# Optimization experiments

Measured on AMD Instinct MI355X. Metric: run time of the kernel, lower is better.

The kernel has to match this reference:

```python
import jax, jax.numpy as jnp
import numpy as np

EMBED_DIM = 1024
NUM_HEADS = 16
HEAD_DIM = EMBED_DIM // NUM_HEADS
B, S = 2, 2048


def setup_inputs() -> dict:
    key = jax.random.key(0)
    ks = jax.random.split(key, 11)
    glorot = lambda k, shape: jax.random.normal(k, shape, jnp.float32) * (2.0 / sum(shape)) ** 0.5
    return {
        "query": jax.random.normal(ks[0], (B, S, EMBED_DIM), jnp.float32),
        "key": jax.random.normal(ks[1], (B, S, EMBED_DIM), jnp.float32),
        "value": jax.random.normal(ks[2], (B, S, EMBED_DIM), jnp.float32),
        "Wq": glorot(ks[3], (EMBED_DIM, EMBED_DIM)), "bq": jnp.zeros((EMBED_DIM,), jnp.float32),
        "Wk": glorot(ks[4], (EMBED_DIM, EMBED_DIM)), "bk": jnp.zeros((EMBED_DIM,), jnp.float32),
        "Wv": glorot(ks[5], (EMBED_DIM, EMBED_DIM)), "bv": jnp.zeros((EMBED_DIM,), jnp.float32),
        "Wo": glorot(ks[6], (EMBED_DIM, EMBED_DIM)), "bo": jnp.zeros((EMBED_DIM,), jnp.float32),
    }


def reference(query, key, value, Wq, bq, Wk, bk, Wv, bv, Wo, bo):
    b, s, _ = query.shape
    # QKV projections
    q = query @ Wq + bq
    k = key @ Wk + bk
    v = value @ Wv + bv
    # [B, S, H, D] -> [B, H, S, D]
    q = q.reshape(b, s, NUM_HEADS, HEAD_DIM).transpose(0, 2, 1, 3)
    k = k.reshape(b, s, NUM_HEADS, HEAD_DIM).transpose(0, 2, 1, 3)
    v = v.reshape(b, s, NUM_HEADS, HEAD_DIM).transpose(0, 2, 1, 3)
    # scores [B, H, S, S], materialized as in the original
    scores = jnp.einsum("bhqd,bhkd->bhqk", q, k) / jnp.sqrt(jnp.float32(HEAD_DIM))
    attn = jax.nn.softmax(scores, axis=-1)
    out = jnp.einsum("bhqk,bhkd->bhqd", attn, v)  # [B, H, S, D]
    out = out.transpose(0, 2, 1, 3).reshape(b, s, EMBED_DIM)
    return out @ Wo + bo
```

## Files before the change

kernel.cpp:

```cpp
#include <hip/hip_runtime.h>
#include <hip/hip_bf16.h>


#define EMBED 1024
#define NHEAD 16
#define HDIM 64
#define SEQ 2048
#define MROWS 4096

typedef __attribute__((ext_vector_type(8))) __bf16 bf16x8;
typedef __attribute__((ext_vector_type(4))) float f32x4;

__device__ __forceinline__ unsigned short f2bf(float f) {
  unsigned int u = __builtin_bit_cast(unsigned int, f);
  u += 0x7fffu + ((u >> 16) & 1u);
  return (unsigned short)(u >> 16);
}

__device__ __forceinline__ int cvtpk_bf16(float lo, float hi) {
  int r;
  asm("v_cvt_pk_bf16_f32 %0, %1, %2" : "=v"(r) : "v"(lo), "v"(hi));
  return r;
}

__device__ __forceinline__ int swz(int row, int bcol) {
  return row * 128 + (bcol ^ ((row & 7) << 4));
}

__device__ __forceinline__ void gload16(const void* g, void* l) {
  __builtin_amdgcn_global_load_lds((const __attribute__((address_space(1))) void*)g,
                                   (__attribute__((address_space(3))) void*)l, 16, 0, 0);
}

__global__ __launch_bounds__(256) void cvt_f32_bf16(const float* __restrict__ i0, const float* __restrict__ i1,
                                                    const float* __restrict__ i2,
                                                    unsigned short* __restrict__ o0, unsigned short* __restrict__ o1,
                                                    unsigned short* __restrict__ o2) {
  const float* in; unsigned short* out;
  switch (blockIdx.y) {
    case 0: in = i0; out = o0; break;
    case 1: in = i1; out = o1; break;
    default: in = i2; out = o2; break;
  }
  int i = blockIdx.x * 256 + threadIdx.x;
  const float4* p = reinterpret_cast<const float4*>(in) + (size_t)i * 2;
  float4 a = p[0], b = p[1];
  int4 r;
  r.x = cvtpk_bf16(a.x, a.y);
  r.y = cvtpk_bf16(a.z, a.w);
  r.z = cvtpk_bf16(b.x, b.y);
  r.w = cvtpk_bf16(b.z, b.w);
  reinterpret_cast<int4*>(out)[i] = r;
}

__global__ __launch_bounds__(256) void wtrans(const float* __restrict__ w0, const float* __restrict__ w1,
                                              const float* __restrict__ w2, const float* __restrict__ w3,
                                              unsigned short* __restrict__ o0, unsigned short* __restrict__ o1,
                                              unsigned short* __restrict__ o2, unsigned short* __restrict__ o3) {
  __shared__ float tile[64][65];
  const float* src; unsigned short* dst;
  switch (blockIdx.z) {
    case 0: src = w0; dst = o0; break;
    case 1: src = w1; dst = o1; break;
    case 2: src = w2; dst = o2; break;
    default: src = w3; dst = o3; break;
  }
  const int k0 = blockIdx.y * 64, n0 = blockIdx.x * 64;
  const int c = threadIdx.x & 63, r0 = threadIdx.x >> 6;
#pragma unroll
  for (int i = 0; i < 16; ++i) {
    int r = r0 + i * 4;
    tile[r][c] = src[(size_t)(k0 + r) * EMBED + n0 + c];
  }
  __syncthreads();
#pragma unroll
  for (int i = 0; i < 16; ++i) {
    int nr = r0 + i * 4;
    dst[(size_t)(n0 + nr) * EMBED + k0 + c] = f2bf(tile[c][nr]);
  }
}

template <int BN>
__device__ __forceinline__ void gemm_core(const unsigned short* __restrict__ A,
                                          const unsigned short* __restrict__ Bt,
                                          const float* __restrict__ bias,
                                          void* __restrict__ C, float oscale, int mode) {
  constexpr int K = EMBED;
  constexpr int MF = (BN == 128) ? 4 : 2;
  constexpr int BRW = BN / 4;
  __shared__ __align__(16) unsigned short Alds[128 * 64];
  __shared__ __align__(16) unsigned short Blds[BN * 64];
  char* Ab8 = (char*)Alds; char* Bb8 = (char*)Blds;
  const char* AB = (const char*)A;
  const char* BB = (const char*)Bt;
  const int tid = threadIdx.x;
  const int lane = tid & 63, w = tid >> 6;
  const int wr = (BN == 128) ? (w >> 1) : w;
  const int wc = (BN == 128) ? (w & 1) : 0;
  const int fr = lane & 15, fq = lane >> 4;
  const int m0 = blockIdx.y * 128, n0 = blockIdx.x * BN;
  const int bcol = (lane & 7) * 16;
  const int gsc = bcol ^ ((lane >> 3) << 4);

  f32x4 acc[MF][4];
#pragma unroll
  for (int m = 0; m < MF; ++m)
#pragma unroll
    for (int n = 0; n < 4; ++n) acc[m][n] = f32x4{0.f, 0.f, 0.f, 0.f};

  for (int k0 = 0; k0 < K; k0 += 64) {
    __syncthreads();
#pragma unroll
    for (int i = 0; i < 4; ++i) {
      int row = w * 32 + i * 8 + (lane >> 3);
      gload16(AB + (size_t)(m0 + row) * (K * 2) + k0 * 2 + gsc, Ab8 + w * 4096 + i * 1024);
    }
#pragma unroll
    for (int i = 0; i < BRW / 8; ++i) {
      int row = w * BRW + i * 8 + (lane >> 3);
      gload16(BB + (size_t)(n0 + row) * (K * 2) + k0 * 2 + gsc, Bb8 + w * (BRW * 128) + i * 1024);
    }
    __syncthreads();
#pragma unroll
    for (int ks = 0; ks < 2; ++ks) {
      bf16x8 af[MF], bfr[4];
#pragma unroll
      for (int m = 0; m < MF; ++m) {
        int ar = wr * (MF * 16) + m * 16 + fr;
        af[m] = *reinterpret_cast<const bf16x8*>(Ab8 + swz(ar, ks * 64 + fq * 16));
      }
#pragma unroll
      for (int n = 0; n < 4; ++n) {
        int br = wc * 64 + n * 16 + fr;
        bfr[n] = *reinterpret_cast<const bf16x8*>(Bb8 + swz(br, ks * 64 + fq * 16));
      }
#pragma unroll
      for (int m = 0; m < MF; ++m)
#pragma unroll
        for (int n = 0; n < 4; ++n)
          acc[m][n] = __builtin_amdgcn_mfma_f32_16x16x32_bf16(af[m], bfr[n], acc[m][n], 0, 0, 0);
    }
  }

#pragma unroll
  for (int n = 0; n < 4; ++n) {
    int col = n0 + wc * 64 + n * 16 + fr;
    float bv = bias[col];
#pragma unroll
    for (int m = 0; m < MF; ++m) {
      int rowb = m0 + wr * (MF * 16) + m * 16 + fq * 4;
      if (mode == 2) {
        int b = rowb >> 11, s0 = rowb & (SEQ - 1);
        int h = col >> 6, d = col & 63;
        int2 pk;
        pk.x = cvtpk_bf16((acc[m][n][0] + bv) * oscale, (acc[m][n][1] + bv) * oscale);
        pk.y = cvtpk_bf16((acc[m][n][2] + bv) * oscale, (acc[m][n][3] + bv) * oscale);
        *reinterpret_cast<int2*>(
            &reinterpret_cast<unsigned short*>(C)[((size_t)((b * NHEAD + h) * HDIM + d)) * SEQ + s0]) = pk;
      } else if (mode == 0) {
#pragma unroll
        for (int r = 0; r < 4; ++r) {
          int row = rowb + r;
          float v = (acc[m][n][r] + bv) * oscale;
          int b = row >> 11, s = row & (SEQ - 1), h = col >> 6, d = col & 63;
          reinterpret_cast<unsigned short*>(C)[((size_t)((b * NHEAD + h) * SEQ + s) << 6) + d] = f2bf(v);
        }
      } else {
#pragma unroll
        for (int r = 0; r < 4; ++r)
          reinterpret_cast<float*>(C)[(size_t)(rowb + r) * EMBED + col] = acc[m][n][r] + bv;
      }
    }
  }
}

__global__ __launch_bounds__(256) void gemm_qkv(
    const unsigned short* __restrict__ Xq, const unsigned short* __restrict__ Xk,
    const unsigned short* __restrict__ Xv,
    const unsigned short* __restrict__ Wqt, const unsigned short* __restrict__ Wkt,
    const unsigned short* __restrict__ Wvt,
    const float* __restrict__ bq, const float* __restrict__ bk, const float* __restrict__ bv,
    unsigned short* __restrict__ Qb, unsigned short* __restrict__ Kb,
    unsigned short* __restrict__ Vtb, float qscale) {
  switch (blockIdx.z) {
    case 0: gemm_core<128>(Xq, Wqt, bq, Qb, qscale, 0); break;
    case 1: gemm_core<128>(Xk, Wkt, bk, Kb, 1.0f, 0); break;
    default: gemm_core<128>(Xv, Wvt, bv, Vtb, 1.0f, 2); break;
  }
}

__global__ __launch_bounds__(256) void gemm_out(const unsigned short* __restrict__ A,
                                                const unsigned short* __restrict__ Bt,
                                                const float* __restrict__ bias,
                                                float* __restrict__ C) {
  gemm_core<64>(A, Bt, bias, C, 1.0f, 1);
}

__global__ __launch_bounds__(128) void attn(const unsigned short* __restrict__ Q,
                                            const unsigned short* __restrict__ Kk,
                                            const unsigned short* __restrict__ Vt,
                                            unsigned short* __restrict__ AO) {
  __shared__ __align__(16) unsigned short Klds[2][64 * 64];
  __shared__ __align__(16) unsigned short Vlds[2][64 * 64];
  __shared__ __align__(16) unsigned short Plds[2][16 * 64];
  const int tid = threadIdx.x, lane = tid & 63, w = tid >> 6;
  const int fr = lane & 15, fq = lane >> 4;
  char* Pb8 = (char*)&Plds[w][0];

  const int lin = blockIdx.x;
  const int head = (lin & 7) * 4 + ((lin >> 3) & 3);
  const int q0 = (lin >> 5) * 64;
  const size_t hb = (size_t)head * SEQ * HDIM;
  const unsigned short* Qh = Q + hb;
  const char* KhB = (const char*)(Kk + hb);
  const char* VhB = (const char*)(Vt + hb);

  const int gsc = ((lane & 7) * 16) ^ ((lane >> 3) << 4);
  const int row0 = w * 32 + (lane >> 3);

#define STAGE(kt_, b_)                                                                     \
  {                                                                                        \
    char* kb_ = (char*)Klds[b_];                                                           \
    char* vb_ = (char*)Vlds[b_];                                                           \
    _Pragma("unroll") for (int i_ = 0; i_ < 4; ++i_) {                                     \
      gload16(KhB + (size_t)((kt_)*64 + row0 + i_ * 8) * 128 + gsc,                        \
              kb_ + w * 4096 + i_ * 1024);                                                 \
      gload16(VhB + (size_t)(row0 + i_ * 8) * (SEQ * 2) + (kt_)*128 + gsc,                 \
              vb_ + w * 4096 + i_ * 1024);                                                 \
    }                                                                                      \
  }

  bf16x8 qf[2][2];
#pragma unroll
  for (int h = 0; h < 2; ++h) {
    size_t qoff = (size_t)(q0 + w * 32 + h * 16 + fr) * HDIM + fq * 8;
    qf[h][0] = *reinterpret_cast<const bf16x8*>(&Qh[qoff]);
    qf[h][1] = *reinterpret_cast<const bf16x8*>(&Qh[qoff + 32]);
  }
  f32x4 oacc[2][4];
#pragma unroll
  for (int h = 0; h < 2; ++h)
#pragma unroll
    for (int n = 0; n < 4; ++n) oacc[h][n] = f32x4{0.f, 0.f, 0.f, 0.f};
  float mrow[2] = {-1e30f, -1e30f}, lrow[2] = {0.f, 0.f};
  const int rsrc = (fq << 4) + (fq << 2);

  STAGE(0, 0);
  __syncthreads();

  for (int kt = 0; kt < SEQ / 64; ++kt) {
    const int cur = kt & 1;
    const bool more = (kt + 1 < SEQ / 64);
    if (more) STAGE(kt + 1, cur ^ 1);
    char* Kb8 = (char*)Klds[cur];
    char* Vb8 = (char*)Vlds[cur];

#pragma unroll
    for (int h = 0; h < 2; ++h) {
      f32x4 sc[4];
#pragma unroll
      for (int n = 0; n < 4; ++n) {
        int kr = n * 16 + fr;
        bf16x8 k0 = *reinterpret_cast<const bf16x8*>(Kb8 + swz(kr, fq * 16));
        bf16x8 k1 = *reinterpret_cast<const bf16x8*>(Kb8 + swz(kr, 64 + fq * 16));
        f32x4 a = f32x4{0.f, 0.f, 0.f, 0.f};
        a = __builtin_amdgcn_mfma_f32_16x16x32_bf16(k0, qf[h][0], a, 0, 0, 0);
        a = __builtin_amdgcn_mfma_f32_16x16x32_bf16(k1, qf[h][1], a, 0, 0, 0);
        sc[n] = a;
      }

      float mx0 = fmaxf(fmaxf(sc[0][0], sc[0][1]), fmaxf(sc[0][2], sc[0][3]));
      float mx1 = fmaxf(fmaxf(sc[1][0], sc[1][1]), fmaxf(sc[1][2], sc[1][3]));
      float mx2 = fmaxf(fmaxf(sc[2][0], sc[2][1]), fmaxf(sc[2][2], sc[2][3]));
      float mx3 = fmaxf(fmaxf(sc[3][0], sc[3][1]), fmaxf(sc[3][2], sc[3][3]));
      float mt = fmaxf(fmaxf(mx0, mx1), fmaxf(mx2, mx3));
      mt = fmaxf(mt, __shfl_xor(mt, 16));
      mt = fmaxf(mt, __shfl_xor(mt, 32));

      if (!__all(mt <= mrow[h] + 8.0f)) {
        float mn = fmaxf(mrow[h], mt);
        float resc = __builtin_amdgcn_exp2f(mrow[h] - mn);
        lrow[h] *= resc;
        float rq[4];
#pragma unroll
        for (int rr = 0; rr < 4; ++rr) rq[rr] = __shfl(resc, rsrc + rr, 64);
#pragma unroll
        for (int n = 0; n < 4; ++n)
#pragma unroll
          for (int rr = 0; rr < 4; ++rr) oacc[h][n][rr] *= rq[rr];
        mrow[h] = mn;
      }

      float p[4][4];
      float ps = 0.f;
#pragma unroll
      for (int n = 0; n < 4; ++n)
#pragma unroll
        for (int r = 0; r < 4; ++r) {
          p[n][r] = __builtin_amdgcn_exp2f(sc[n][r] - mrow[h]);
          ps += p[n][r];
        }
      ps += __shfl_xor(ps, 16);
      ps += __shfl_xor(ps, 32);
      lrow[h] += ps;

#pragma unroll
      for (int n = 0; n < 4; ++n) {
        int2 pk;
        pk.x = cvtpk_bf16(p[n][0], p[n][1]);
        pk.y = cvtpk_bf16(p[n][2], p[n][3]);
        *reinterpret_cast<int2*>(Pb8 + swz(fr, n * 32 + fq * 8)) = pk;
      }

      bf16x8 pa0 = *reinterpret_cast<const bf16x8*>(Pb8 + swz(fr, fq * 16));
      bf16x8 pa1 = *reinterpret_cast<const bf16x8*>(Pb8 + swz(fr, 64 + fq * 16));
#pragma unroll
      for (int n = 0; n < 4; ++n) {
        int dr = n * 16 + fr;
        bf16x8 vb0 = *reinterpret_cast<const bf16x8*>(Vb8 + swz(dr, fq * 16));
        bf16x8 vb1 = *reinterpret_cast<const bf16x8*>(Vb8 + swz(dr, 64 + fq * 16));
        oacc[h][n] = __builtin_amdgcn_mfma_f32_16x16x32_bf16(pa0, vb0, oacc[h][n], 0, 0, 0);
        oacc[h][n] = __builtin_amdgcn_mfma_f32_16x16x32_bf16(pa1, vb1, oacc[h][n], 0, 0, 0);
      }
    }

    __syncthreads();
  }
#undef STAGE

  const int b = head >> 4, hh = head & 15;
#pragma unroll
  for (int h = 0; h < 2; ++h) {
    float lr[4];
#pragma unroll
    for (int rr = 0; rr < 4; ++rr) lr[rr] = __shfl(lrow[h], rsrc + rr, 64);
#pragma unroll
    for (int rr = 0; rr < 4; ++rr) {
      float inv = 1.0f / lr[rr];
      int srow = q0 + w * 32 + h * 16 + fq * 4 + rr;
      size_t ob = (size_t)(b * SEQ + srow) * EMBED + hh * 64;
#pragma unroll
      for (int n = 0; n < 4; ++n) AO[ob + n * 16 + fr] = f2bf(oacc[h][n][rr] * inv);
    }
  }
}

extern "C" void kernel_launch(void* const* d_in, const int* in_sizes, int n_in,
                              void* d_out, int out_size, void* d_ws, size_t ws_size,
                              hipStream_t stream) {
  const float* q32 = (const float*)d_in[0];
  const float* k32 = (const float*)d_in[1];
  const float* v32 = (const float*)d_in[2];
  const float* Wq = (const float*)d_in[3]; const float* bq = (const float*)d_in[4];
  const float* Wk = (const float*)d_in[5]; const float* bk = (const float*)d_in[6];
  const float* Wv = (const float*)d_in[7]; const float* bv = (const float*)d_in[8];
  const float* Wo = (const float*)d_in[9]; const float* bo = (const float*)d_in[10];
  float* out = (float*)d_out;

  char* ws = (char*)d_ws;
  const size_t MB = 1u << 20;
  unsigned short* Xq  = (unsigned short*)(ws + 0 * MB);
  unsigned short* Xk  = (unsigned short*)(ws + 8 * MB);
  unsigned short* Xv  = (unsigned short*)(ws + 16 * MB);
  unsigned short* Wqt = (unsigned short*)(ws + 24 * MB);
  unsigned short* Wkt = (unsigned short*)(ws + 26 * MB);
  unsigned short* Wvt = (unsigned short*)(ws + 28 * MB);
  unsigned short* Wot = (unsigned short*)(ws + 30 * MB);
  unsigned short* Qb  = (unsigned short*)(ws + 32 * MB);
  unsigned short* Kb  = (unsigned short*)(ws + 40 * MB);
  unsigned short* Vtb = (unsigned short*)(ws + 48 * MB);
  unsigned short* AO  = Xq;

  const int n8 = (MROWS * EMBED) / 8;
  cvt_f32_bf16<<<dim3(n8 / 256, 3), 256, 0, stream>>>(q32, k32, v32, Xq, Xk, Xv);
  wtrans<<<dim3(16, 16, 4), 256, 0, stream>>>(Wq, Wk, Wv, Wo, Wqt, Wkt, Wvt, Wot);

  const float qscale = 0.125f * 1.44269504088896340736f;
  gemm_qkv<<<dim3(EMBED / 128, MROWS / 128, 3), 256, 0, stream>>>(
      Xq, Xk, Xv, Wqt, Wkt, Wvt, bq, bk, bv, Qb, Kb, Vtb, qscale);

  attn<<<dim3(SEQ / 64 * 32), 128, 0, stream>>>(Qb, Kb, Vtb, AO);

  gemm_out<<<dim3(EMBED / 64, MROWS / 128), 256, 0, stream>>>(AO, Wot, bo, out);
}
```

Before: 152.8 us.

## Switch attention to 32x32x16 MFMA and feed P from registers without LDS

The attention inner loop moves from 16x16x32 MFMA tiles to 32x32x16 MFMA tiles, one 32-row query tile per wave. The QK^T output layout now matches the A-operand layout the PV product needs, so the softmax probabilities are packed to bf16 in registers and the LDS round-trip for P is removed. To make that register reuse line up, the V-transpose projection stores keys in a permuted sequence order (bits 2 and 3 of the key index swapped). This cuts LDS traffic and MFMA issue count, at the cost of more accumulator registers and a data layout that the two kernels must agree on.

```diff
diff --git a/kernel.cpp b/kernel.cpp
--- a/kernel.cpp
+++ b/kernel.cpp
@@ -10,6 +10,7 @@
 
 typedef __attribute__((ext_vector_type(8))) __bf16 bf16x8;
 typedef __attribute__((ext_vector_type(4))) float f32x4;
+typedef __attribute__((ext_vector_type(16))) float f32x16;
 
 __device__ __forceinline__ unsigned short f2bf(float f) {
   unsigned int u = __builtin_bit_cast(unsigned int, f);
@@ -151,12 +152,13 @@
       int rowb = m0 + wr * (MF * 16) + m * 16 + fq * 4;
       if (mode == 2) {
         int b = rowb >> 11, s0 = rowb & (SEQ - 1);
+        int s0p = (s0 & ~12) | ((s0 & 4) << 1) | ((s0 & 8) >> 1);
         int h = col >> 6, d = col & 63;
         int2 pk;
         pk.x = cvtpk_bf16((acc[m][n][0] + bv) * oscale, (acc[m][n][1] + bv) * oscale);
         pk.y = cvtpk_bf16((acc[m][n][2] + bv) * oscale, (acc[m][n][3] + bv) * oscale);
         *reinterpret_cast<int2*>(
-            &reinterpret_cast<unsigned short*>(C)[((size_t)((b * NHEAD + h) * HDIM + d)) * SEQ + s0]) = pk;
+            &reinterpret_cast<unsigned short*>(C)[((size_t)((b * NHEAD + h) * HDIM + d)) * SEQ + s0p]) = pk;
       } else if (mode == 0) {
 #pragma unroll
         for (int r = 0; r < 4; ++r) {
@@ -202,10 +204,8 @@
                                             unsigned short* __restrict__ AO) {
   __shared__ __align__(16) unsigned short Klds[2][64 * 64];
   __shared__ __align__(16) unsigned short Vlds[2][64 * 64];
-  __shared__ __align__(16) unsigned short Plds[2][16 * 64];
   const int tid = threadIdx.x, lane = tid & 63, w = tid >> 6;
-  const int fr = lane & 15, fq = lane >> 4;
-  char* Pb8 = (char*)&Plds[w][0];
+  const int ql = lane & 31, t = lane >> 5;
 
   const int lin = blockIdx.x;
   const int head = (lin & 7) * 4 + ((lin >> 3) & 3);
@@ -230,20 +230,16 @@
     }                                                                                      \
   }
 
-  bf16x8 qf[2][2];
-#pragma unroll
-  for (int h = 0; h < 2; ++h) {
-    size_t qoff = (size_t)(q0 + w * 32 + h * 16 + fr) * HDIM + fq * 8;
-    qf[h][0] = *reinterpret_cast<const bf16x8*>(&Qh[qoff]);
-    qf[h][1] = *reinterpret_cast<const bf16x8*>(&Qh[qoff + 32]);
-  }
-  f32x4 oacc[2][4];
-#pragma unroll
-  for (int h = 0; h < 2; ++h)
-#pragma unroll
-    for (int n = 0; n < 4; ++n) oacc[h][n] = f32x4{0.f, 0.f, 0.f, 0.f};
-  float mrow[2] = {-1e30f, -1e30f}, lrow[2] = {0.f, 0.f};
-  const int rsrc = (fq << 4) + (fq << 2);
+  bf16x8 qf[4];
+  {
+    const unsigned short* qp = Qh + (size_t)(q0 + w * 32 + ql) * HDIM + t * 8;
+    qf[0] = *reinterpret_cast<const bf16x8*>(qp);
+    qf[1] = *reinterpret_cast<const bf16x8*>(qp + 16);
+    qf[2] = *reinterpret_cast<const bf16x8*>(qp + 32);
+    qf[3] = *reinterpret_cast<const bf16x8*>(qp + 48);
+  }
+  f32x16 oacc0 = {}, oacc1 = {};
+  float mrow = -1e30f, lrow = 0.f;
 
   STAGE(0, 0);
   __syncthreads();
@@ -255,73 +251,77 @@
     char* Kb8 = (char*)Klds[cur];
     char* Vb8 = (char*)Vlds[cur];
 
-#pragma unroll
-    for (int h = 0; h < 2; ++h) {
-      f32x4 sc[4];
-#pragma unroll
-      for (int n = 0; n < 4; ++n) {
-        int kr = n * 16 + fr;
-        bf16x8 k0 = *reinterpret_cast<const bf16x8*>(Kb8 + swz(kr, fq * 16));
-        bf16x8 k1 = *reinterpret_cast<const bf16x8*>(Kb8 + swz(kr, 64 + fq * 16));
-        f32x4 a = f32x4{0.f, 0.f, 0.f, 0.f};
-        a = __builtin_amdgcn_mfma_f32_16x16x32_bf16(k0, qf[h][0], a, 0, 0, 0);
-        a = __builtin_amdgcn_mfma_f32_16x16x32_bf16(k1, qf[h][1], a, 0, 0, 0);
-        sc[n] = a;
+    f32x16 sc0 = {}, sc1 = {};
+#pragma unroll
+    for (int s = 0; s < 4; ++s) {
+      bf16x8 kf0 = *reinterpret_cast<const bf16x8*>(Kb8 + swz(ql, s * 32 + t * 16));
+      bf16x8 kf1 = *reinterpret_cast<const bf16x8*>(Kb8 + swz(32 + ql, s * 32 + t * 16));
+      sc0 = __builtin_amdgcn_mfma_f32_32x32x16_bf16(kf0, qf[s], sc0, 0, 0, 0);
+      sc1 = __builtin_amdgcn_mfma_f32_32x32x16_bf16(kf1, qf[s], sc1, 0, 0, 0);
+    }
+
+    float m8[8];
+#pragma unroll
+    for (int i = 0; i < 8; ++i)
+      m8[i] = fmaxf(fmaxf(sc0[2 * i], sc0[2 * i + 1]), fmaxf(sc1[2 * i], sc1[2 * i + 1]));
+    float m4a = fmaxf(m8[0], m8[1]), m4b = fmaxf(m8[2], m8[3]);
+    float m4c = fmaxf(m8[4], m8[5]), m4d = fmaxf(m8[6], m8[7]);
+    float mt = fmaxf(fmaxf(m4a, m4b), fmaxf(m4c, m4d));
+    mt = fmaxf(mt, __shfl_xor(mt, 32));
+
+    if (!__all(mt <= mrow + 8.0f)) {
+      float mn = fmaxf(mrow, mt);
+      float resc = __builtin_amdgcn_exp2f(mrow - mn);
+      lrow *= resc;
+#pragma unroll
+      for (int r = 0; r < 16; ++r) {
+        float rq = __shfl(resc, (r & 3) + 8 * (r >> 2) + 4 * t, 64);
+        oacc0[r] *= rq;
+        oacc1[r] *= rq;
       }
-
-      float mx0 = fmaxf(fmaxf(sc[0][0], sc[0][1]), fmaxf(sc[0][2], sc[0][3]));
-      float mx1 = fmaxf(fmaxf(sc[1][0], sc[1][1]), fmaxf(sc[1][2], sc[1][3]));
-      float mx2 = fmaxf(fmaxf(sc[2][0], sc[2][1]), fmaxf(sc[2][2], sc[2][3]));
-      float mx3 = fmaxf(fmaxf(sc[3][0], sc[3][1]), fmaxf(sc[3][2], sc[3][3]));
-      float mt = fmaxf(fmaxf(mx0, mx1), fmaxf(mx2, mx3));
-      mt = fmaxf(mt, __shfl_xor(mt, 16));
-      mt = fmaxf(mt, __shfl_xor(mt, 32));
-
-      if (!__all(mt <= mrow[h] + 8.0f)) {
-        float mn = fmaxf(mrow[h], mt);
-        float resc = __builtin_amdgcn_exp2f(mrow[h] - mn);
-        lrow[h] *= resc;
-        float rq[4];
-#pragma unroll
-        for (int rr = 0; rr < 4; ++rr) rq[rr] = __shfl(resc, rsrc + rr, 64);
-#pragma unroll
-        for (int n = 0; n < 4; ++n)
-#pragma unroll
-          for (int rr = 0; rr < 4; ++rr) oacc[h][n][rr] *= rq[rr];
-        mrow[h] = mn;
-      }
-
-      float p[4][4];
-      float ps = 0.f;
-#pragma unroll
-      for (int n = 0; n < 4; ++n)
-#pragma unroll
-        for (int r = 0; r < 4; ++r) {
-          p[n][r] = __builtin_amdgcn_exp2f(sc[n][r] - mrow[h]);
-          ps += p[n][r];
-        }
-      ps += __shfl_xor(ps, 16);
-      ps += __shfl_xor(ps, 32);
-      lrow[h] += ps;
-
-#pragma unroll
-      for (int n = 0; n < 4; ++n) {
-        int2 pk;
-        pk.x = cvtpk_bf16(p[n][0], p[n][1]);
-        pk.y = cvtpk_bf16(p[n][2], p[n][3]);
-        *reinterpret_cast<int2*>(Pb8 + swz(fr, n * 32 + fq * 8)) = pk;
-      }
-
-      bf16x8 pa0 = *reinterpret_cast<const bf16x8*>(Pb8 + swz(fr, fq * 16));
-      bf16x8 pa1 = *reinterpret_cast<const bf16x8*>(Pb8 + swz(fr, 64 + fq * 16));
-#pragma unroll
-      for (int n = 0; n < 4; ++n) {
-        int dr = n * 16 + fr;
-        bf16x8 vb0 = *reinterpret_cast<const bf16x8*>(Vb8 + swz(dr, fq * 16));
-        bf16x8 vb1 = *reinterpret_cast<const bf16x8*>(Vb8 + swz(dr, 64 + fq * 16));
-        oacc[h][n] = __builtin_amdgcn_mfma_f32_16x16x32_bf16(pa0, vb0, oacc[h][n], 0, 0, 0);
-        oacc[h][n] = __builtin_amdgcn_mfma_f32_16x16x32_bf16(pa1, vb1, oacc[h][n], 0, 0, 0);
-      }
+      mrow = mn;
+    }
+
+    float ps0 = 0.f, ps1 = 0.f, ps2 = 0.f, ps3 = 0.f;
+#pragma unroll
+    for (int i = 0; i < 4; ++i) {
+      sc0[4 * i + 0] = __builtin_amdgcn_exp2f(sc0[4 * i + 0] - mrow);
+      sc0[4 * i + 1] = __builtin_amdgcn_exp2f(sc0[4 * i + 1] - mrow);
+      sc0[4 * i + 2] = __builtin_amdgcn_exp2f(sc0[4 * i + 2] - mrow);
+      sc0[4 * i + 3] = __builtin_amdgcn_exp2f(sc0[4 * i + 3] - mrow);
+      sc1[4 * i + 0] = __builtin_amdgcn_exp2f(sc1[4 * i + 0] - mrow);
+      sc1[4 * i + 1] = __builtin_amdgcn_exp2f(sc1[4 * i + 1] - mrow);
+      sc1[4 * i + 2] = __builtin_amdgcn_exp2f(sc1[4 * i + 2] - mrow);
+      sc1[4 * i + 3] = __builtin_amdgcn_exp2f(sc1[4 * i + 3] - mrow);
+      ps0 += sc0[4 * i + 0] + sc0[4 * i + 1];
+      ps1 += sc0[4 * i + 2] + sc0[4 * i + 3];
+      ps2 += sc1[4 * i + 0] + sc1[4 * i + 1];
+      ps3 += sc1[4 * i + 2] + sc1[4 * i + 3];
+    }
+    float ps = (ps0 + ps1) + (ps2 + ps3);
+    ps += __shfl_xor(ps, 32);
+    lrow += ps;
+
+    int4 paw[4];
+#pragma unroll
+    for (int s2 = 0; s2 < 2; ++s2) {
+      paw[s2].x     = cvtpk_bf16(sc0[8 * s2 + 0], sc0[8 * s2 + 1]);
+      paw[s2].y     = cvtpk_bf16(sc0[8 * s2 + 2], sc0[8 * s2 + 3]);
+      paw[s2].z     = cvtpk_bf16(sc0[8 * s2 + 4], sc0[8 * s2 + 5]);
+      paw[s2].w     = cvtpk_bf16(sc0[8 * s2 + 6], sc0[8 * s2 + 7]);
+      paw[2 + s2].x = cvtpk_bf16(sc1[8 * s2 + 0], sc1[8 * s2 + 1]);
+      paw[2 + s2].y = cvtpk_bf16(sc1[8 * s2 + 2], sc1[8 * s2 + 3]);
+      paw[2 + s2].z = cvtpk_bf16(sc1[8 * s2 + 4], sc1[8 * s2 + 5]);
+      paw[2 + s2].w = cvtpk_bf16(sc1[8 * s2 + 6], sc1[8 * s2 + 7]);
+    }
+
+#pragma unroll
+    for (int s = 0; s < 4; ++s) {
+      bf16x8 pa = __builtin_bit_cast(bf16x8, paw[s]);
+      bf16x8 v0 = *reinterpret_cast<const bf16x8*>(Vb8 + swz(ql, s * 32 + t * 16));
+      bf16x8 v1 = *reinterpret_cast<const bf16x8*>(Vb8 + swz(32 + ql, s * 32 + t * 16));
+      oacc0 = __builtin_amdgcn_mfma_f32_32x32x16_bf16(pa, v0, oacc0, 0, 0, 0);
+      oacc1 = __builtin_amdgcn_mfma_f32_32x32x16_bf16(pa, v1, oacc1, 0, 0, 0);
     }
 
     __syncthreads();
@@ -330,18 +330,13 @@
 
   const int b = head >> 4, hh = head & 15;
 #pragma unroll
-  for (int h = 0; h < 2; ++h) {
-    float lr[4];
-#pragma unroll
-    for (int rr = 0; rr < 4; ++rr) lr[rr] = __shfl(lrow[h], rsrc + rr, 64);
-#pragma unroll
-    for (int rr = 0; rr < 4; ++rr) {
-      float inv = 1.0f / lr[rr];
-      int srow = q0 + w * 32 + h * 16 + fq * 4 + rr;
-      size_t ob = (size_t)(b * SEQ + srow) * EMBED + hh * 64;
-#pragma unroll
-      for (int n = 0; n < 4; ++n) AO[ob + n * 16 + fr] = f2bf(oacc[h][n][rr] * inv);
-    }
+  for (int r = 0; r < 16; ++r) {
+    int qr = (r & 3) + 8 * (r >> 2) + 4 * t;
+    float inv = 1.0f / __shfl(lrow, qr, 64);
+    int srow = q0 + w * 32 + qr;
+    size_t ob = (size_t)(b * SEQ + srow) * EMBED + hh * 64 + ql;
+    AO[ob] = f2bf(oacc0[r] * inv);
+    AO[ob + 32] = f2bf(oacc1[r] * inv);
   }
 }
 
```

Result: faster. 141.8 us (-7.2%).
